# Kernel optimization log

Hardware: AMD Instinct MI355X
Metric: run time of the kernel (lower is better)

## Reference

```python
import jax, jax.numpy as jnp
import numpy as np

# Lorentz hyperboloid with curvature -1 (k = 1): <x,x>_L = -1/k, x0 = time coord.
K_CURV = 1.0
EPS = 1e-8
B, N, D, H = 4, 1024, 1024, 16
HD = D // H  # dim_per_head = 64 (space dims per head)


def _time(space):
    # time coord so the point lies on the hyperboloid
    return jnp.sqrt(jnp.sum(space * space, axis=-1, keepdims=True) + 1.0 / K_CURV)


def _lift(space):
    return jnp.concatenate([_time(space), space], axis=-1)


def _linner(u, v):
    # Minkowski inner product <u,v>_L = -u0 v0 + u_s . v_s
    return jnp.sum(u[..., 1:] * v[..., 1:], axis=-1) - u[..., 0] * v[..., 0]


def _lorentz_layernorm(x, gamma, beta):
    s = x[..., 1:]
    mu = jnp.mean(s, axis=-1, keepdims=True)
    var = jnp.mean((s - mu) ** 2, axis=-1, keepdims=True)
    s = (s - mu) / jnp.sqrt(var + 1e-5) * gamma + beta
    return _lift(s)


def _lorentz_linear(x, W, b):
    # linear on the full Lorentz point -> space part of output, time recomputed
    return _lift(x @ W + b)


def _lresnet(x, y, w):
    # Lorentzian residual: (x + w*y) renormalized back onto the hyperboloid
    z = x + w * y
    denom = jnp.sqrt(jnp.clip(-_linner(z, z), EPS))[..., None]
    return z / (jnp.sqrt(K_CURV) * denom)


def _attention(x, Wq, bq, Wk, bk, Wv, bv, Wo, bo):
    def heads(W, b):
        s = (x @ W + b).reshape(B, N, H, HD).transpose(0, 2, 1, 3)  # [B,H,N,HD]
        return _lift(s)  # per-head Lorentz points [B,H,N,HD+1]

    q, k, v = heads(Wq, bq), heads(Wk, bk), heads(Wv, bv)
    sgn = jnp.concatenate([-jnp.ones((1,), x.dtype), jnp.ones((HD,), x.dtype)])
    # pairwise Minkowski inner products; score = -d_L^2 = 2/k + 2<q,k>_L, scaled
    scores = jnp.einsum('bhqd,bhkd->bhqk', q * sgn, k)
    scores = (2.0 / K_CURV + 2.0 * scores) / np.sqrt(HD).astype(np.float32)
    attn = jax.nn.softmax(scores, axis=-1)
    # Lorentz midpoint aggregation of values
    mid = jnp.einsum('bhqk,bhkd->bhqd', attn, v)
    denom = jnp.sqrt(jnp.clip(-_linner(mid, mid), EPS))[..., None]
    mid = mid / (jnp.sqrt(K_CURV) * denom)  # [B,H,N,HD+1]
    cat = mid.transpose(0, 2, 1, 3).reshape(B, N, H * (HD + 1))  # trans_heads_concat
    return _lift(cat @ Wo + bo)


def reference(x, g1, b1, Wq, bq, Wk, bk, Wv, bv, Wo, bo, g2, b2, Wfc, bfc, Wpj, bpj, w1, w2):
    lx = _lorentz_layernorm(x, g1, b1)
    ax = _attention(lx, Wq, bq, Wk, bk, Wv, bv, Wo, bo)
    x = _lresnet(x, ax, w1)
    h = _lorentz_layernorm(x, g2, b2)
    h = _lorentz_linear(h, Wfc, bfc)                      # [B,N,4D]
    h = _lift(jax.nn.gelu(h[..., 1:], approximate=False))  # LorentzActivation(GELU)
    h = _lorentz_linear(h, Wpj, bpj)                      # [B,N,D]
    return _lresnet(x, h, w2)


def setup_inputs() -> dict:
    key = jax.random.key(0)
    ks = jax.random.split(key, 8)
    sc = 0.02
    f32 = jnp.float32
    xs = jax.random.normal(ks[0], (B, N, D - 1), f32)
    return dict(
        x=_lift(xs),
        g1=jnp.ones((D - 1,), f32), b1=jnp.zeros((D - 1,), f32),
        Wq=sc * jax.random.normal(ks[1], (D, H * HD), f32), bq=jnp.zeros((H * HD,), f32),
        Wk=sc * jax.random.normal(ks[2], (D, H * HD), f32), bk=jnp.zeros((H * HD,), f32),
        Wv=sc * jax.random.normal(ks[3], (D, H * HD), f32), bv=jnp.zeros((H * HD,), f32),
        Wo=sc * jax.random.normal(ks[4], (H * (HD + 1), D - 1), f32), bo=jnp.zeros((D - 1,), f32),
        g2=jnp.ones((D - 1,), f32), b2=jnp.zeros((D - 1,), f32),
        Wfc=sc * jax.random.normal(ks[5], (D, 4 * D - 1), f32), bfc=jnp.zeros((4 * D - 1,), f32),
        Wpj=sc * jax.random.normal(ks[6], (4 * D, D - 1), f32), bpj=jnp.zeros((D - 1,), f32),
        w1=jnp.ones((), f32), w2=jnp.ones((), f32),
    )
```

## Files before the change

kernel.cpp:

```cpp
#include <hip/hip_runtime.h>
#include <math.h>

#define BB 4
#define NN 1024
#define DD 1024
#define HH 16
#define ROWS (BB*NN)

typedef __attribute__((ext_vector_type(8))) short bf16x8;
typedef __attribute__((ext_vector_type(4))) float f32x4;
typedef __attribute__((ext_vector_type(4))) unsigned short u16x4;
typedef __attribute__((ext_vector_type(8))) unsigned short u16x8;
typedef unsigned short u16;

__device__ __forceinline__ u16 f2bf(float f) {
    union { float f; unsigned u; } v; v.f = f;
    unsigned r = v.u + 0x7fff + ((v.u >> 16) & 1);
    return (u16)(r >> 16);
}
__device__ __forceinline__ float bf2f(u16 u) {
    union { unsigned u; float f; } v; v.u = ((unsigned)u) << 16; return v.f;
}

__device__ __forceinline__ void async16(const void* g, void* l) {
    __builtin_amdgcn_global_load_lds(
        (__attribute__((address_space(1))) void*)(uintptr_t)g,
        (__attribute__((address_space(3))) void*)(uintptr_t)l,
        16, 0, 0);
}

__device__ __forceinline__ float block_reduce_sum(float v, float* sm) {
    #pragma unroll
    for (int o = 32; o > 0; o >>= 1) v += __shfl_down(v, o);
    int lane = threadIdx.x & 63, wid = threadIdx.x >> 6;
    if (lane == 0) sm[wid] = v;
    __syncthreads();
    if (wid == 0) {
        v = (lane < (int)(blockDim.x >> 6)) ? sm[lane] : 0.f;
        #pragma unroll
        for (int o = 2; o > 0; o >>= 1) v += __shfl_down(v, o);
        if (lane == 0) sm[0] = v;
    }
    __syncthreads();
    float r = sm[0];
    __syncthreads();
    return r;
}

__device__ __forceinline__ void block_reduce3(float& a, float& b, float& c, float* sm) {
    #pragma unroll
    for (int o = 32; o > 0; o >>= 1) {
        a += __shfl_down(a, o); b += __shfl_down(b, o); c += __shfl_down(c, o);
    }
    int lane = threadIdx.x & 63, wid = threadIdx.x >> 6;
    if (lane == 0) { sm[wid] = a; sm[8 + wid] = b; sm[16 + wid] = c; }
    __syncthreads();
    int nw = (int)(blockDim.x >> 6);
    if (wid == 0) {
        float va = (lane < nw) ? sm[lane] : 0.f;
        float vb = (lane < nw) ? sm[8 + lane] : 0.f;
        float vc = (lane < nw) ? sm[16 + lane] : 0.f;
        #pragma unroll
        for (int o = 2; o > 0; o >>= 1) {
            va += __shfl_down(va, o); vb += __shfl_down(vb, o); vc += __shfl_down(vc, o);
        }
        if (lane == 0) { sm[0] = va; sm[8] = vb; sm[16] = vc; }
    }
    __syncthreads();
    a = sm[0]; b = sm[8]; c = sm[16];
    __syncthreads();
}

__global__ __launch_bounds__(256) void k_pre(
        const float* __restrict__ Wq_, const float* __restrict__ Wk_,
        const float* __restrict__ Wv_, const float* __restrict__ Wo_,
        const float* __restrict__ Wfc_, const float* __restrict__ Wpj_,
        u16* __restrict__ WqkvT, u16* __restrict__ WoT,
        u16* __restrict__ WfcT, u16* __restrict__ WpjT,
        const float* __restrict__ x, const float* __restrict__ g1,
        const float* __restrict__ be1, u16* __restrict__ lnout) {
    __shared__ float t[32][33];
    int bid = blockIdx.x;
    if (bid < 12352) {
        const float* W; u16* out; int K, N, Kpad, Npad, gx;
        if (bid < 1024)      { W = Wq_;  out = WqkvT;            K = 1024; N = 1024; Kpad = 1024; Npad = 1024; gx = 32; }
        else if (bid < 2048) { W = Wk_;  out = WqkvT + 1048576;  K = 1024; N = 1024; Kpad = 1024; Npad = 1024; gx = 32; bid -= 1024; }
        else if (bid < 3072) { W = Wv_;  out = WqkvT + 2097152;  K = 1024; N = 1024; Kpad = 1024; Npad = 1024; gx = 32; bid -= 2048; }
        else if (bid < 4160) { W = Wo_;  out = WoT;              K = 1040; N = 1023; Kpad = 1088; Npad = 1024; gx = 34; bid -= 3072; }
        else if (bid < 8256) { W = Wfc_; out = WfcT;             K = 1024; N = 4095; Kpad = 1024; Npad = 4096; gx = 32; bid -= 4160; }
        else                 { W = Wpj_; out = WpjT;             K = 4096; N = 1023; Kpad = 4096; Npad = 1024; gx = 128; bid -= 8256; }
        int k0 = (bid % gx) * 32, n0 = (bid / gx) * 32;
        int tx = threadIdx.x & 31, ty = threadIdx.x >> 5;
        #pragma unroll
        for (int i = 0; i < 32; i += 8) {
            int k = k0 + ty + i, n = n0 + tx;
            t[ty + i][tx] = (k < K && n < N) ? W[(size_t)k * N + n] : 0.f;
        }
        __syncthreads();
        #pragma unroll
        for (int i = 0; i < 32; i += 8) {
            int n = n0 + ty + i, k = k0 + tx;
            if (n < Npad && k < Kpad) out[(size_t)n * Kpad + k] = f2bf(t[tx][ty + i]);
        }
    } else {
        float* sm = &t[0][0];
        int row = bid - 12352, tid = threadIdx.x;
        const float4* xr4 = (const float4*)(x + (size_t)row * DD);
        float4 xv = xr4[tid];
        float s = 0.f, ss = 0.f, dummy = 0.f;
        #pragma unroll
        for (int e = 0; e < 4; ++e) {
            if (tid | e) {
                float v = ((const float*)&xv)[e];
                s += v; ss += v * v;
            }
        }
        block_reduce3(s, ss, dummy, sm);
        float mu = s * (1.f / 1023.f);
        float var = ss * (1.f / 1023.f) - mu * mu;
        float rstd = rsqrtf(var + 1e-5f);
        float vo[4]; float s2 = 0.f;
        #pragma unroll
        for (int e = 0; e < 4; ++e) {
            int c = 4 * tid + e;
            if (c > 0) {
                float v = (((const float*)&xv)[e] - mu) * rstd * g1[c - 1] + be1[c - 1];
                vo[e] = v; s2 += v * v;
            } else vo[e] = 0.f;
        }
        s2 = block_reduce_sum(s2, sm);
        u16x4 lo;
        #pragma unroll
        for (int e = 0; e < 4; ++e) lo[e] = f2bf(vo[e]);
        if (tid == 0) lo[0] = f2bf(sqrtf(s2 + 1.f));
        ((u16x4*)(lnout + (size_t)row * DD))[tid] = lo;
    }
}

__device__ __forceinline__ void cstore(float* p, float v) { *p = v; }
__device__ __forceinline__ void cstore(u16* p, float v) { *p = f2bf(v); }

template <typename OT>
__global__ __launch_bounds__(256) void k_gemm_mfma(
        const u16* __restrict__ A, const u16* __restrict__ BT,
        const float* __restrict__ bias, int nbias,
        OT* __restrict__ C0, OT* __restrict__ C1,
        int ldc, int ldab, int ksplit, int K) {
    __shared__ __align__(16) u16 As[2][128 * 64];
    __shared__ __align__(16) u16 Bs[2][128 * 64];
    int z = blockIdx.z;
    int kbeg = z ? ksplit : 0;
    int kend = z ? K : ksplit;
    OT* C = z ? C1 : C0;
    const float* bs = z ? nullptr : bias;

    int tid = threadIdx.x;
    int wave = tid >> 6, lane = tid & 63;
    int quad = lane >> 4, m16 = lane & 15;
    int n0 = blockIdx.x * 128, m0 = blockIdx.y * 128;
    int wm = (wave & 1) * 64, wn = (wave >> 1) * 64;

    f32x4 acc[4][4];
    #pragma unroll
    for (int t = 0; t < 4; ++t)
        #pragma unroll
        for (int u = 0; u < 4; ++u) acc[t][u] = (f32x4){0.f, 0.f, 0.f, 0.f};

    int r8 = lane >> 3;
    int cc = (lane & 7) ^ r8;
    int srow = wave * 32 + r8;
    const u16* ag = A  + (size_t)(m0 + srow) * ldab + cc * 8;
    const u16* bg = BT + (size_t)(n0 + srow) * ldab + cc * 8;

    auto stage = [&](int k0, int s) {
        #pragma unroll
        for (int j = 0; j < 4; ++j) {
            async16(ag + (size_t)(j * 8) * ldab + k0, &As[s][(wave * 32 + j * 8) * 64]);
            async16(bg + (size_t)(j * 8) * ldab + k0, &Bs[s][(wave * 32 + j * 8) * 64]);
        }
    };

    int niter = (kend - kbeg) >> 6;
    stage(kbeg, 0);
    for (int it = 0; it < niter; ++it) {
        int cur = it & 1;
        __syncthreads();
        if (it + 1 < niter) stage(kbeg + (it + 1) * 64, cur ^ 1);
        #pragma unroll
        for (int kk = 0; kk < 2; ++kk) {
            bf16x8 af[4], bfr[4];
            #pragma unroll
            for (int t = 0; t < 4; ++t) {
                int slot = (kk * 4 + quad) ^ (m16 & 7);
                af[t] = *(const bf16x8*)&As[cur][(wm + t * 16 + m16) * 64 + slot * 8];
            }
            #pragma unroll
            for (int u = 0; u < 4; ++u) {
                int slot = (kk * 4 + quad) ^ (m16 & 7);
                bfr[u] = *(const bf16x8*)&Bs[cur][(wn + u * 16 + m16) * 64 + slot * 8];
            }
            #pragma unroll
            for (int t = 0; t < 4; ++t)
                #pragma unroll
                for (int u = 0; u < 4; ++u)
                    acc[t][u] = __builtin_amdgcn_mfma_f32_16x16x32_bf16(af[t], bfr[u], acc[t][u], 0, 0, 0);
        }
    }
    #pragma unroll
    for (int u = 0; u < 4; ++u) {
        int col = n0 + wn + u * 16 + m16;
        if (col < nbias) {
            float bv = (bs != nullptr) ? bs[col] : 0.f;
            #pragma unroll
            for (int t = 0; t < 4; ++t) {
                #pragma unroll
                for (int r = 0; r < 4; ++r) {
                    int row = m0 + wm + t * 16 + quad * 4 + r;
                    cstore(C + (size_t)row * ldc + col, acc[t][u][r] + bv);
                }
            }
        }
    }
}

__global__ __launch_bounds__(256) void k_gemm_qkv(
        const u16* __restrict__ A, const u16* __restrict__ BT,
        const float* __restrict__ bq, const float* __restrict__ bk,
        const float* __restrict__ bv,
        u16* __restrict__ Qp, u16* __restrict__ Kp, u16* __restrict__ V2) {
    __shared__ __align__(16) u16 As[2][128 * 64];
    __shared__ __align__(16) u16 Bs[2][128 * 64];
    int tid = threadIdx.x;
    int wave = tid >> 6, lane = tid & 63;
    int quad = lane >> 4, m16 = lane & 15;
    int n0 = blockIdx.x * 128, m0 = blockIdx.y * 128;
    int wm = (wave & 1) * 64, wn = (wave >> 1) * 64;

    f32x4 acc[4][4];
    #pragma unroll
    for (int t = 0; t < 4; ++t)
        #pragma unroll
        for (int u = 0; u < 4; ++u) acc[t][u] = (f32x4){0.f, 0.f, 0.f, 0.f};

    int r8 = lane >> 3;
    int cc = (lane & 7) ^ r8;
    int srow = wave * 32 + r8;
    const u16* ag = A  + (size_t)(m0 + srow) * 1024 + cc * 8;
    const u16* bg = BT + (size_t)(n0 + srow) * 1024 + cc * 8;

    auto stage = [&](int k0, int s) {
        #pragma unroll
        for (int j = 0; j < 4; ++j) {
            async16(ag + (size_t)(j * 8) * 1024 + k0, &As[s][(wave * 32 + j * 8) * 64]);
            async16(bg + (size_t)(j * 8) * 1024 + k0, &Bs[s][(wave * 32 + j * 8) * 64]);
        }
    };

    stage(0, 0);
    for (int it = 0; it < 16; ++it) {
        int cur = it & 1;
        __syncthreads();
        if (it + 1 < 16) stage((it + 1) * 64, cur ^ 1);
        #pragma unroll
        for (int kk = 0; kk < 2; ++kk) {
            bf16x8 af[4], bfr[4];
            #pragma unroll
            for (int t = 0; t < 4; ++t) {
                int slot = (kk * 4 + quad) ^ (m16 & 7);
                af[t] = *(const bf16x8*)&As[cur][(wm + t * 16 + m16) * 64 + slot * 8];
            }
            #pragma unroll
            for (int u = 0; u < 4; ++u) {
                int slot = (kk * 4 + quad) ^ (m16 & 7);
                bfr[u] = *(const bf16x8*)&Bs[cur][(wn + u * 16 + m16) * 64 + slot * 8];
            }
            #pragma unroll
            for (int t = 0; t < 4; ++t)
                #pragma unroll
                for (int u = 0; u < 4; ++u)
                    acc[t][u] = __builtin_amdgcn_mfma_f32_16x16x32_bf16(af[t], bfr[u], acc[t][u], 0, 0, 0);
        }
    }

    int sec = n0 >> 10;
    int h = ((n0 & 1023) + wn) >> 6;
    int b = m0 >> 10;
    int b16h = b * 16 + h;
    const float* bias = (sec == 0) ? bq : (sec == 1) ? bk : bv;
    float bvu[4];
    #pragma unroll
    for (int u = 0; u < 4; ++u) bvu[u] = bias[h * 64 + u * 16 + m16];

    if (sec < 2) {
        const int strd = (sec == 0) ? 96 : 104;
        u16* P = (sec == 0) ? Qp : Kp;
        const float tsign = (sec == 0) ? -1.f : 1.f;
        #pragma unroll
        for (int t = 0; t < 4; ++t) {
            #pragma unroll
            for (int r = 0; r < 4; ++r) {
                int n = (m0 + wm + t * 16 + quad * 4 + r) & 1023;
                u16* drow = P + ((size_t)b16h * 1024 + n) * strd;
                float vv[4]; float ss = 0.f;
                #pragma unroll
                for (int u = 0; u < 4; ++u) { vv[u] = acc[t][u][r] + bvu[u]; ss += vv[u] * vv[u]; }
                ss += __shfl_xor(ss, 1); ss += __shfl_xor(ss, 2);
                ss += __shfl_xor(ss, 4); ss += __shfl_xor(ss, 8);
                #pragma unroll
                for (int u = 0; u < 4; ++u) drow[1 + u * 16 + m16] = f2bf(vv[u]);
                if (m16 == 0) drow[0] = f2bf(tsign * sqrtf(ss + 1.f));
                drow[65 + m16] = 0;
                if (m16 < 15) drow[81 + m16] = 0;
            }
        }
    } else {
        int tile = ((m0 & 1023) + wm) >> 6;
        size_t tbase = ((size_t)b16h * 16 + tile) * 6144;
        #pragma unroll
        for (int t = 0; t < 4; ++t) {
            int tok0 = t * 16 + quad * 4;
            u16x4 tc;
            u16x4 pk[4];
            #pragma unroll
            for (int r = 0; r < 4; ++r) {
                float vv[4]; float ss = 0.f;
                #pragma unroll
                for (int u = 0; u < 4; ++u) { vv[u] = acc[t][u][r] + bvu[u]; ss += vv[u] * vv[u]; }
                ss += __shfl_xor(ss, 1); ss += __shfl_xor(ss, 2);
                ss += __shfl_xor(ss, 4); ss += __shfl_xor(ss, 8);
                tc[r] = f2bf(sqrtf(ss + 1.f));
                #pragma unroll
                for (int u = 0; u < 4; ++u) pk[u][r] = f2bf(vv[u]);
            }
            #pragma unroll
            for (int u = 0; u < 4; ++u) {
                int d = u * 16 + m16;
                *(u16x4*)&V2[tbase + (size_t)(1 + d) * 72 + tok0] = pk[u];
            }
            if (m16 == 0) *(u16x4*)&V2[tbase + tok0] = tc;
        }
        for (int i = lane; i < 240; i += 64) {
            int rr = 65 + (i >> 4), sg = (i & 15) << 2;
            *(u16x4*)&V2[tbase + (size_t)rr * 72 + sg] = (u16x4){0, 0, 0, 0};
        }
    }
}

#define AKS 104
#define AVS 72
#define APS 88
#define KTILE_U16 (64 * AKS)
#define VTILE_U16 6144
#define EXPC 0.36067376f
__global__ __launch_bounds__(512) void k_attn_mfma(
        const u16* __restrict__ Qp, const u16* __restrict__ Kp,
        const u16* __restrict__ V2, u16* __restrict__ cat) {
    __shared__ __align__(16) u16 Klds[2][KTILE_U16];
    __shared__ __align__(16) u16 Vlds[2][VTILE_U16];
    __shared__ __align__(16) u16 Plds[8][16 * APS];
    int tid = threadIdx.x;
    int wave = tid >> 6, lane = tid & 63;
    int quad = lane >> 4, m = lane & 15;
    int wq = wave & 3, g = wave >> 2;
    int bid = blockIdx.x;
    int bh = ((bid & 7) << 3) | (bid >> 6);
    int qt = (bid >> 3) & 7;

    const u16* kg = Kp + (size_t)bh * 16 * KTILE_U16;
    const u16* vg = V2 + (size_t)bh * 16 * VTILE_U16;

    bf16x8 aq[3];
    {
        const u16* qptr = Qp + ((size_t)bh * 1024 + qt * 128 + g * 64 + wq * 16 + m) * 96;
        aq[0] = *(const bf16x8*)(qptr + quad * 8);
        aq[1] = *(const bf16x8*)(qptr + 32 + quad * 8);
        aq[2] = *(const bf16x8*)(qptr + 64 + quad * 8);
    }

    f32x4 O[5];
    #pragma unroll
    for (int i = 0; i < 5; ++i) O[i] = (f32x4){0.f, 0.f, 0.f, 0.f};

    auto stage = [&](int kt, int s) {
        const u16* kt_p = kg + kt * KTILE_U16 + lane * 8;
        const u16* vt_p = vg + kt * VTILE_U16 + lane * 8;
        for (int i = wave; i < 25; i += 8) {
            if (i < 13) async16(kt_p + i * 512, &Klds[s][i * 512]);
            else        async16(vt_p + (i - 13) * 512, &Vlds[s][(i - 13) * 512]);
        }
    };

    stage(0, 0);
    for (int kt = 0; kt < 16; ++kt) {
        int cur = kt & 1;
        __syncthreads();
        if (kt < 15) stage(kt + 1, cur ^ 1);
        u16* pw = &Plds[wave][0];
        #pragma unroll
        for (int nt = 0; nt < 4; ++nt) {
            f32x4 acc = (f32x4){0.f, 0.f, 0.f, 0.f};
            const u16* kr = &Klds[cur][(nt * 16 + m) * AKS + quad * 8];
            acc = __builtin_amdgcn_mfma_f32_16x16x32_bf16(*(const bf16x8*)(kr),      aq[0], acc, 0, 0, 0);
            acc = __builtin_amdgcn_mfma_f32_16x16x32_bf16(*(const bf16x8*)(kr + 32), aq[1], acc, 0, 0, 0);
            acc = __builtin_amdgcn_mfma_f32_16x16x32_bf16(*(const bf16x8*)(kr + 64), aq[2], acc, 0, 0, 0);
            unsigned pk0, pk1;
            {
                union { float f; unsigned u; } a0, a1, a2, a3;
                a0.f = __builtin_amdgcn_exp2f(fmaf(acc[0], EXPC, EXPC));
                a1.f = __builtin_amdgcn_exp2f(fmaf(acc[1], EXPC, EXPC));
                a2.f = __builtin_amdgcn_exp2f(fmaf(acc[2], EXPC, EXPC));
                a3.f = __builtin_amdgcn_exp2f(fmaf(acc[3], EXPC, EXPC));
                pk0 = ((a0.u + 0x8000u) >> 16) | (((a1.u + 0x8000u) >> 16) << 16);
                pk1 = ((a2.u + 0x8000u) >> 16) | (((a3.u + 0x8000u) >> 16) << 16);
            }
            uint2 pk; pk.x = pk0; pk.y = pk1;
            *(uint2*)&pw[m * APS + nt * 16 + quad * 4] = pk;
        }
        #pragma unroll
        for (int kc = 0; kc < 2; ++kc) {
            bf16x8 ap = *(const bf16x8*)&Plds[wave][m * APS + kc * 32 + quad * 8];
            #pragma unroll
            for (int vt = 0; vt < 5; ++vt) {
                bf16x8 bv = *(const bf16x8*)&Vlds[cur][(vt * 16 + m) * AVS + kc * 32 + quad * 8];
                O[vt] = __builtin_amdgcn_mfma_f32_16x16x32_bf16(ap, bv, O[vt], 0, 0, 0);
            }
        }
    }
    int b = bh >> 4, h = bh & 15;
    #pragma unroll
    for (int r = 0; r < 4; ++r) {
        float part = 0.f;
        #pragma unroll
        for (int vt = 0; vt < 5; ++vt) {
            int c = vt * 16 + m;
            float o = O[vt][r];
            part += (c == 0) ? o * o : -o * o;
        }
        part += __shfl_xor(part, 1);
        part += __shfl_xor(part, 2);
        part += __shfl_xor(part, 4);
        part += __shfl_xor(part, 8);
        float rden = rsqrtf(fmaxf(part, 1e-8f));
        int n = qt * 128 + g * 64 + wq * 16 + quad * 4 + r;
        u16* crow = cat + (size_t)(b * 1024 + n) * 1088 + h * 65;
        #pragma unroll
        for (int vt = 0; vt < 5; ++vt) {
            int c = vt * 16 + m;
            if (c < 65) crow[c] = f2bf(O[vt][r] * rden);
        }
    }
    if (h == 15) {
        for (int i = tid; i < 128 * 48; i += 512) {
            int rr = i / 48, c = i - rr * 48;
            int n = qt * 128 + rr;
            cat[(size_t)(b * 1024 + n) * 1088 + 1040 + c] = 0;
        }
    }
}

__global__ __launch_bounds__(256) void k_lresnet_ln(
        const float* __restrict__ x, const float* __restrict__ y0,
        const float* __restrict__ y1, const float* __restrict__ wscale,
        const float* __restrict__ g2, const float* __restrict__ be2,
        float* __restrict__ x1, u16* __restrict__ lnout) {
    __shared__ float sm[24];
    int row = blockIdx.x, tid = threadIdx.x;
    float w = *wscale;
    float4 xv = ((const float4*)(x  + (size_t)row * DD))[tid];
    float4 av = ((const float4*)(y0 + (size_t)row * 1024))[tid];
    float4 bv = ((const float4*)(y1 + (size_t)row * 1024))[tid];
    float zv[4];
    float sy = 0.f, sz = 0.f, szs = 0.f;
    #pragma unroll
    for (int e = 0; e < 4; ++e) {
        float y = ((const float*)&av)[e] + ((const float*)&bv)[e];
        float z = ((const float*)&xv)[e] + w * y;
        zv[e] = z;
        if (tid | e) { sy += y * y; sz += z * z; szs += z; }
    }
    block_reduce3(sy, sz, szs, sm);
    float x0 = x[(size_t)row * DD];
    float z0 = x0 + w * sqrtf(sy + 1.f);
    float q = z0 * z0 - sz;
    float rden = rsqrtf(fmaxf(q, 1e-8f));
    float mu = rden * szs * (1.f / 1023.f);
    float ex2 = rden * rden * sz * (1.f / 1023.f);
    float rstd = rsqrtf(ex2 - mu * mu + 1e-5f);
    float4 xo; float vo[4]; float s2 = 0.f;
    #pragma unroll
    for (int e = 0; e < 4; ++e) {
        int c = 4 * tid + e;
        float xn = zv[e] * rden;
        ((float*)&xo)[e] = xn;
        if (c > 0) {
            float v = (xn - mu) * rstd * g2[c - 1] + be2[c - 1];
            vo[e] = v; s2 += v * v;
        } else vo[e] = 0.f;
    }
    if (tid == 0) ((float*)&xo)[0] = z0 * rden;
    ((float4*)(x1 + (size_t)row * DD))[tid] = xo;
    s2 = block_reduce_sum(s2, sm);
    u16x4 lo;
    #pragma unroll
    for (int e = 0; e < 4; ++e) lo[e] = f2bf(vo[e]);
    if (tid == 0) lo[0] = f2bf(sqrtf(s2 + 1.f));
    ((u16x4*)(lnout + (size_t)row * DD))[tid] = lo;
}

__global__ __launch_bounds__(256) void k_lresnet(
        const float* __restrict__ x, const float* __restrict__ y0,
        const float* __restrict__ y1, const float* __restrict__ wscale,
        float* __restrict__ out) {
    __shared__ float sm[24];
    int row = blockIdx.x, tid = threadIdx.x;
    float w = *wscale;
    float4 xv = ((const float4*)(x  + (size_t)row * DD))[tid];
    float4 av = ((const float4*)(y0 + (size_t)row * 1024))[tid];
    float4 bv = ((const float4*)(y1 + (size_t)row * 1024))[tid];
    float zv[4];
    float sy = 0.f, sz = 0.f, dummy = 0.f;
    #pragma unroll
    for (int e = 0; e < 4; ++e) {
        float y = ((const float*)&av)[e] + ((const float*)&bv)[e];
        float z = ((const float*)&xv)[e] + w * y;
        zv[e] = z;
        if (tid | e) { sy += y * y; sz += z * z; }
    }
    block_reduce3(sy, sz, dummy, sm);
    float x0 = x[(size_t)row * DD];
    float z0 = x0 + w * sqrtf(sy + 1.f);
    float q = z0 * z0 - sz;
    float rden = rsqrtf(fmaxf(q, 1e-8f));
    float4 o;
    #pragma unroll
    for (int e = 0; e < 4; ++e) ((float*)&o)[e] = zv[e] * rden;
    if (tid == 0) ((float*)&o)[0] = z0 * rden;
    ((float4*)(out + (size_t)row * DD))[tid] = o;
}

__global__ __launch_bounds__(256) void k_gelu_lift(
        const u16* __restrict__ hfc, u16* __restrict__ hg) {
    __shared__ float sm[8];
    int row = blockIdx.x, tid = threadIdx.x;
    const u16* hr = hfc + (size_t)row * 4096;
    u16* gr = hg + (size_t)row * 4096;
    float s2 = 0.f;
    #pragma unroll
    for (int p = 0; p < 2; ++p) {
        int c = (tid + 256 * p) * 8;
        u16x8 hv = *(const u16x8*)(hr + c);
        u16x8 ov;
        #pragma unroll
        for (int e = 0; e < 8; ++e) {
            float gl;
            if (c + e == 0) gl = 0.f;
            else {
                float v = bf2f(hv[e]);
                gl = 0.5f * v * (1.f + erff(v * 0.70710678f));
                s2 += gl * gl;
            }
            ov[e] = f2bf(gl);
        }
        *(u16x8*)(gr + c) = ov;
    }
    s2 = block_reduce_sum(s2, sm);
    if (tid == 0) gr[0] = f2bf(sqrtf(s2 + 1.f));
}

extern "C" void kernel_launch(void* const* d_in, const int* in_sizes, int n_in,
                              void* d_out, int out_size, void* d_ws, size_t ws_size,
                              hipStream_t stream) {
    const float* x   = (const float*)d_in[0];
    const float* g1  = (const float*)d_in[1];
    const float* b1  = (const float*)d_in[2];
    const float* Wq  = (const float*)d_in[3];
    const float* bq  = (const float*)d_in[4];
    const float* Wk  = (const float*)d_in[5];
    const float* bk  = (const float*)d_in[6];
    const float* Wv  = (const float*)d_in[7];
    const float* bv  = (const float*)d_in[8];
    const float* Wo  = (const float*)d_in[9];
    const float* bo  = (const float*)d_in[10];
    const float* g2  = (const float*)d_in[11];
    const float* b2  = (const float*)d_in[12];
    const float* Wfc = (const float*)d_in[13];
    const float* bfc = (const float*)d_in[14];
    const float* Wpj = (const float*)d_in[15];
    const float* bpj = (const float*)d_in[16];
    const float* w1  = (const float*)d_in[17];
    const float* w2  = (const float*)d_in[18];
    float* out = (float*)d_out;

    char* W = (char*)d_ws;
    u16* lx_bf  = (u16*)(W + 0);
    u16* WqkvT  = (u16*)(W + 8388608);
    u16* WoT    = (u16*)(W + 14680064);
    u16* WfcT   = (u16*)(W + 16908288);
    u16* WpjT   = (u16*)(W + 25296896);
    u16* Qp     = (u16*)(W + 58851328);
    u16* Kp     = (u16*)(W + 71434240);
    u16* V2     = (u16*)(W + 85065728);
    u16* cat_bf = (u16*)(W + 97648640);
    float* ax0  = (float*)(W + 33685504);
    float* ax1  = (float*)(W + 50462720);
    float* x1   = (float*)(W + 67239936);
    u16* hfc_bf = (u16*)(W + 84017152);
    u16* hg_bf  = (u16*)(W + 33685504);
    float* h2a  = (float*)(W + 84017152);
    float* h2b  = (float*)(W + 100794368);

    dim3 blk(256);

    k_pre<<<16448, blk, 0, stream>>>(Wq, Wk, Wv, Wo, Wfc, Wpj,
                                     WqkvT, WoT, WfcT, WpjT,
                                     x, g1, b1, lx_bf);

    k_gemm_qkv<<<dim3(24, 32, 1), blk, 0, stream>>>(
        lx_bf, WqkvT, bq, bk, bv, Qp, Kp, V2);

    k_attn_mfma<<<512, dim3(512), 0, stream>>>(Qp, Kp, V2, cat_bf);

    k_gemm_mfma<float><<<dim3(8, 32, 2), blk, 0, stream>>>(
        cat_bf, WoT, bo, 1023, ax0 + 1, ax1 + 1, 1024, 1088, 576, 1088);

    k_lresnet_ln<<<ROWS, blk, 0, stream>>>(x, ax0, ax1, w1, g2, b2, x1, lx_bf);

    k_gemm_mfma<u16><<<dim3(32, 32, 1), blk, 0, stream>>>(
        lx_bf, WfcT, bfc, 4095, hfc_bf + 1, hfc_bf + 1, 4096, 1024, 1024, 1024);

    k_gelu_lift<<<ROWS, blk, 0, stream>>>(hfc_bf, hg_bf);

    k_gemm_mfma<float><<<dim3(8, 32, 2), blk, 0, stream>>>(
        hg_bf, WpjT, bpj, 1023, h2a + 1, h2b + 1, 1024, 4096, 2048, 4096);

    k_lresnet<<<ROWS, blk, 0, stream>>>(x1, h2a, h2b, w2, out);
}
```

Baseline: 401.8 us.

## Align GEMM output stores and remap block order for split-K GEMMs

GEMM outputs are now written at aligned base pointers instead of offset by one element. The consuming elementwise kernels shift values by one position through a shared-memory edge exchange between neighbouring threads. The aim is to remove misaligned stores from the GEMM epilogue. A block-index swizzle is also added to the two split-K float GEMMs, regrouping row tiles to improve L2 locality. The cost is an extra LDS exchange and barrier in each row kernel.

```diff
diff --git a/kernel.cpp b/kernel.cpp
--- a/kernel.cpp
+++ b/kernel.cpp
@@ -145,7 +145,7 @@
         const u16* __restrict__ A, const u16* __restrict__ BT,
         const float* __restrict__ bias, int nbias,
         OT* __restrict__ C0, OT* __restrict__ C1,
-        int ldc, int ldab, int ksplit, int K) {
+        int ldc, int ldab, int ksplit, int K, int swz) {
     __shared__ __align__(16) u16 As[2][128 * 64];
     __shared__ __align__(16) u16 Bs[2][128 * 64];
     int z = blockIdx.z;
@@ -154,10 +154,20 @@
     OT* C = z ? C1 : C0;
     const float* bs = z ? nullptr : bias;
 
+    int bx = blockIdx.x, by = blockIdx.y;
+    if (swz) {
+        int nx = gridDim.x, ny = gridDim.y;
+        int flat = bx + nx * by;
+        int c = flat & 7, i = flat >> 3;
+        int hi = i / nx;
+        by = c * (ny >> 3) + hi;
+        bx = i - hi * nx;
+    }
+
     int tid = threadIdx.x;
     int wave = tid >> 6, lane = tid & 63;
     int quad = lane >> 4, m16 = lane & 15;
-    int n0 = blockIdx.x * 128, m0 = blockIdx.y * 128;
+    int n0 = bx * 128, m0 = by * 128;
     int wm = (wave & 1) * 64, wn = (wave >> 1) * 64;
 
     f32x4 acc[4][4];
@@ -464,19 +474,29 @@
         const float* __restrict__ g2, const float* __restrict__ be2,
         float* __restrict__ x1, u16* __restrict__ lnout) {
     __shared__ float sm[24];
+    __shared__ float edge[256];
     int row = blockIdx.x, tid = threadIdx.x;
     float w = *wscale;
     float4 xv = ((const float4*)(x  + (size_t)row * DD))[tid];
     float4 av = ((const float4*)(y0 + (size_t)row * 1024))[tid];
     float4 bv = ((const float4*)(y1 + (size_t)row * 1024))[tid];
+    float yv[4];
+    #pragma unroll
+    for (int e = 0; e < 4; ++e) yv[e] = ((const float*)&av)[e] + ((const float*)&bv)[e];
+    edge[tid] = yv[3];
+    float sy = 0.f;
+    #pragma unroll
+    for (int e = 0; e < 4; ++e) if (4 * tid + e < 1023) sy += yv[e] * yv[e];
+    __syncthreads();
+    float yprev = tid ? edge[tid - 1] : 0.f;
     float zv[4];
-    float sy = 0.f, sz = 0.f, szs = 0.f;
+    float sz = 0.f, szs = 0.f;
     #pragma unroll
     for (int e = 0; e < 4; ++e) {
-        float y = ((const float*)&av)[e] + ((const float*)&bv)[e];
-        float z = ((const float*)&xv)[e] + w * y;
+        float yc = (e == 0) ? yprev : yv[e - 1];
+        float z = ((const float*)&xv)[e] + w * yc;
         zv[e] = z;
-        if (tid | e) { sy += y * y; sz += z * z; szs += z; }
+        if (tid | e) { sz += z * z; szs += z; }
     }
     block_reduce3(sy, sz, szs, sm);
     float x0 = x[(size_t)row * DD];
@@ -512,19 +532,29 @@
         const float* __restrict__ y1, const float* __restrict__ wscale,
         float* __restrict__ out) {
     __shared__ float sm[24];
+    __shared__ float edge[256];
     int row = blockIdx.x, tid = threadIdx.x;
     float w = *wscale;
     float4 xv = ((const float4*)(x  + (size_t)row * DD))[tid];
     float4 av = ((const float4*)(y0 + (size_t)row * 1024))[tid];
     float4 bv = ((const float4*)(y1 + (size_t)row * 1024))[tid];
+    float yv[4];
+    #pragma unroll
+    for (int e = 0; e < 4; ++e) yv[e] = ((const float*)&av)[e] + ((const float*)&bv)[e];
+    edge[tid] = yv[3];
+    float sy = 0.f;
+    #pragma unroll
+    for (int e = 0; e < 4; ++e) if (4 * tid + e < 1023) sy += yv[e] * yv[e];
+    __syncthreads();
+    float yprev = tid ? edge[tid - 1] : 0.f;
     float zv[4];
-    float sy = 0.f, sz = 0.f, dummy = 0.f;
+    float sz = 0.f, dummy = 0.f;
     #pragma unroll
     for (int e = 0; e < 4; ++e) {
-        float y = ((const float*)&av)[e] + ((const float*)&bv)[e];
-        float z = ((const float*)&xv)[e] + w * y;
+        float yc = (e == 0) ? yprev : yv[e - 1];
+        float z = ((const float*)&xv)[e] + w * yc;
         zv[e] = z;
-        if (tid | e) { sy += y * y; sz += z * z; }
+        if (tid | e) sz += z * z;
     }
     block_reduce3(sy, sz, dummy, sm);
     float x0 = x[(size_t)row * DD];
@@ -541,28 +571,39 @@
 __global__ __launch_bounds__(256) void k_gelu_lift(
         const u16* __restrict__ hfc, u16* __restrict__ hg) {
     __shared__ float sm[8];
+    __shared__ u16 edge[512];
     int row = blockIdx.x, tid = threadIdx.x;
     const u16* hr = hfc + (size_t)row * 4096;
     u16* gr = hg + (size_t)row * 4096;
+    u16x8 hv0 = *(const u16x8*)(hr + tid * 8);
+    u16x8 hv1 = *(const u16x8*)(hr + 2048 + tid * 8);
+    edge[tid] = hv0[7];
+    edge[256 + tid] = hv1[7];
+    __syncthreads();
+    u16 p0 = tid ? edge[tid - 1] : (u16)0;
+    u16 p1 = edge[255 + tid];
     float s2 = 0.f;
-    #pragma unroll
-    for (int p = 0; p < 2; ++p) {
-        int c = (tid + 256 * p) * 8;
-        u16x8 hv = *(const u16x8*)(hr + c);
-        u16x8 ov;
-        #pragma unroll
-        for (int e = 0; e < 8; ++e) {
-            float gl;
-            if (c + e == 0) gl = 0.f;
-            else {
-                float v = bf2f(hv[e]);
-                gl = 0.5f * v * (1.f + erff(v * 0.70710678f));
-                s2 += gl * gl;
-            }
-            ov[e] = f2bf(gl);
-        }
-        *(u16x8*)(gr + c) = ov;
-    }
+    u16x8 ov0, ov1;
+    #pragma unroll
+    for (int e = 0; e < 8; ++e) {
+        int c = 8 * tid + e;
+        float gl = 0.f;
+        if (c > 0) {
+            float v = bf2f((e == 0) ? p0 : hv0[e - 1]);
+            gl = 0.5f * v * (1.f + erff(v * 0.70710678f));
+            s2 += gl * gl;
+        }
+        ov0[e] = f2bf(gl);
+    }
+    #pragma unroll
+    for (int e = 0; e < 8; ++e) {
+        float v = bf2f((e == 0) ? p1 : hv1[e - 1]);
+        float gl = 0.5f * v * (1.f + erff(v * 0.70710678f));
+        s2 += gl * gl;
+        ov1[e] = f2bf(gl);
+    }
+    *(u16x8*)(gr + tid * 8) = ov0;
+    *(u16x8*)(gr + 2048 + tid * 8) = ov1;
     s2 = block_reduce_sum(s2, sm);
     if (tid == 0) gr[0] = f2bf(sqrtf(s2 + 1.f));
 }
@@ -621,17 +662,17 @@
     k_attn_mfma<<<512, dim3(512), 0, stream>>>(Qp, Kp, V2, cat_bf);
 
     k_gemm_mfma<float><<<dim3(8, 32, 2), blk, 0, stream>>>(
-        cat_bf, WoT, bo, 1023, ax0 + 1, ax1 + 1, 1024, 1088, 576, 1088);
+        cat_bf, WoT, bo, 1023, ax0, ax1, 1024, 1088, 576, 1088, 1);
 
     k_lresnet_ln<<<ROWS, blk, 0, stream>>>(x, ax0, ax1, w1, g2, b2, x1, lx_bf);
 
     k_gemm_mfma<u16><<<dim3(32, 32, 1), blk, 0, stream>>>(
-        lx_bf, WfcT, bfc, 4095, hfc_bf + 1, hfc_bf + 1, 4096, 1024, 1024, 1024);
+        lx_bf, WfcT, bfc, 4095, hfc_bf, hfc_bf, 4096, 1024, 1024, 1024, 0);
 
     k_gelu_lift<<<ROWS, blk, 0, stream>>>(hfc_bf, hg_bf);
 
     k_gemm_mfma<float><<<dim3(8, 32, 2), blk, 0, stream>>>(
-        hg_bf, WpjT, bpj, 1023, h2a + 1, h2b + 1, 1024, 4096, 2048, 4096);
+        hg_bf, WpjT, bpj, 1023, h2a, h2b, 1024, 4096, 2048, 4096, 1);
 
     k_lresnet<<<ROWS, blk, 0, stream>>>(x1, h2a, h2b, w2, out);
 }
```

Measured after the change: 377.1 us. 6.2% less time.
